# Optimization experiments

Hardware: AMD Instinct MI355X
Metric: run time of the kernel (lower is better)

The kernel has to match this reference:

```python
import jax, jax.numpy as jnp
import numpy as np

B, N, HID, H, DH, NB = 4, 4096, 768, 12, 64, 266
EPS = 1e-4


def softmax_kernel(data, proj, is_query):
    # data: [B,H,N,DH], proj: [NB,DH]. FAVOR+ positive softmax features.
    d = data.shape[-1]
    ratio = proj.shape[0] ** -0.5
    dn = d ** -0.25  # data normalizer
    data_dash = jnp.einsum('bhnd,jd->bhnj', data * dn, proj)  # [B,H,N,NB]
    diag = 0.5 * jnp.sum((data * dn) ** 2, axis=-1, keepdims=True)  # [B,H,N,1]
    if is_query:
        m = jnp.max(data_dash, axis=-1, keepdims=True)
    else:
        m = jnp.max(data_dash, axis=(-1, -2), keepdims=True)
    return ratio * (jnp.exp(data_dash - diag - m) + EPS)


def setup_inputs() -> dict:
    key = jax.random.key(0)
    ks = jax.random.split(key, 8)
    s = HID ** -0.5
    return {
        'hidden_states': jax.random.normal(ks[0], (B, N, HID), jnp.float32),
        'Wq': jax.random.normal(ks[1], (HID, HID), jnp.float32) * s,
        'bq': jnp.zeros((HID,), jnp.float32),
        'Wk': jax.random.normal(ks[2], (HID, HID), jnp.float32) * s,
        'bk': jnp.zeros((HID,), jnp.float32),
        'Wv': jax.random.normal(ks[3], (HID, HID), jnp.float32) * s,
        'bv': jnp.zeros((HID,), jnp.float32),
        'proj': jax.random.normal(ks[4], (NB, DH), jnp.float32),
    }


def reference(hidden_states, Wq, bq, Wk, bk, Wv, bv, proj):
    def heads(x):  # [B,N,HID] -> [B,H,N,DH]
        return x.reshape(B, N, H, DH).transpose(0, 2, 1, 3)

    q = heads(hidden_states @ Wq.T + bq)
    k = heads(hidden_states @ Wk.T + bk)
    v = heads(hidden_states @ Wv.T + bv)

    qp = softmax_kernel(q, proj, True)   # [B,H,N,NB]
    kp = softmax_kernel(k, proj, False)  # [B,H,N,NB]

    # non-causal linear attention: out = q' (k'^T v) / (q' sum_n k')
    k_sum = jnp.sum(kp, axis=2)                               # [B,H,NB]
    d_inv = 1.0 / jnp.einsum('bhnj,bhj->bhn', qp, k_sum)      # [B,H,N]
    ctx = jnp.einsum('bhnj,bhnd->bhjd', kp, v)                # [B,H,NB,DH]
    out = jnp.einsum('bhnj,bhjd->bhnd', qp, ctx) * d_inv[..., None]

    return out.transpose(0, 2, 1, 3).reshape(B, N, HID)
```

## Files before the change

kernel.cpp:

```cpp
#include <hip/hip_runtime.h>
#include <hip/hip_bf16.h>
#include <stdint.h>

#define B_   4
#define N_   4096
#define HID_ 768
#define H_   12
#define DH_  64
#define NB_  266
#define NBP_ 288
#define EPS_ 1e-4f
#define RATIO_ 0.06131393f

typedef unsigned short u16;
typedef __attribute__((ext_vector_type(8))) short short8;
typedef __attribute__((ext_vector_type(4))) float floatx4;

__device__ __forceinline__ u16 f2b(float f) {
  __hip_bfloat16 h = __float2bfloat16(f);
  return *reinterpret_cast<u16*>(&h);
}
__device__ __forceinline__ float b2f(u16 u) {
  union { unsigned u; float f; } x; x.u = ((unsigned)u) << 16; return x.f;
}
__device__ __forceinline__ unsigned fmap(float x) {
  unsigned u = __float_as_uint(x);
  return (u & 0x80000000u) ? ~u : (u | 0x80000000u);
}
__device__ __forceinline__ float funmap(unsigned u) {
  unsigned b = (u & 0x80000000u) ? (u & 0x7FFFFFFFu) : ~u;
  return __uint_as_float(b);
}
__device__ __forceinline__ void gl16(const u16* g, u16* l) {
  __builtin_amdgcn_global_load_lds(
      (const __attribute__((address_space(1))) void*)g,
      (__attribute__((address_space(3))) void*)l, 16, 0, 0);
}

__global__ __launch_bounds__(256) void k_prep(
    const float4* __restrict__ hs, const float4* __restrict__ Wq,
    const float4* __restrict__ Wk, const float4* __restrict__ Wv,
    const float* __restrict__ proj,
    uint2* __restrict__ hsb, uint2* __restrict__ wb3, u16* __restrict__ projb,
    unsigned* __restrict__ mbuf) {
  int blk = blockIdx.x;
  const int t = threadIdx.x;
  if (blk < 12288) {
    int i = blk * 256 + t;
    float4 v = hs[i];
    union { u16 s[4]; uint2 u; } pk;
    pk.s[0] = f2b(v.x); pk.s[1] = f2b(v.y); pk.s[2] = f2b(v.z); pk.s[3] = f2b(v.w);
    hsb[i] = pk.u;
    return;
  }
  blk -= 12288;
  if (blk < 1728) {
    int i = blk * 256 + t;
    int sel = i / 147456, j = i - sel * 147456;
    const float4* s = (sel == 0) ? Wq : (sel == 1) ? Wk : Wv;
    float4 v = s[j];
    union { u16 s4[4]; uint2 u; } pk;
    pk.s4[0] = f2b(v.x); pk.s4[1] = f2b(v.y); pk.s4[2] = f2b(v.z); pk.s4[3] = f2b(v.w);
    wb3[i] = pk.u;
    return;
  }
  blk -= 1728;
  if (blk < 72) {
    int i = blk * 256 + t;
    int j = i / DH_, d = i - j * DH_;
    float v = (j < NB_) ? proj[j * DH_ + d] * 0.35355339059327373f : 0.f;
    projb[i] = f2b(v);
    return;
  }
  blk -= 72;
  if (blk == 0 && t < B_ * H_) mbuf[t] = 0u;
}

__global__ __launch_bounds__(512, 2) void k_qkv2(
    const u16* __restrict__ hsb, const u16* __restrict__ wb,
    const float* __restrict__ bq, const float* __restrict__ bk, const float* __restrict__ bv,
    u16* __restrict__ qb, u16* __restrict__ kb, u16* __restrict__ vT) {
  __shared__ u16 lds[3 * 16384];
  const int orig = blockIdx.x;
  const int lg = (orig & 7) * 72 + (orig >> 3);
  const int tm = lg / 9, tn = lg - tm * 9;
  const int m0 = tm * 256;
  const int c0 = tn * 256;
  const int sel = c0 / 768;
  const int or0 = c0 - sel * 768;
  const u16* W = wb + (size_t)sel * HID_ * HID_;
  const int t = threadIdx.x, lane = t & 63, wv = t >> 6;
  const int lm = lane & 15, lq = lane >> 4;
  const int wvm = wv >> 2, wvn = wv & 3;
  const int srow = t >> 2;
  const int scol = ((t & 3) ^ ((t >> 3) & 3)) * 8;
  const u16* gA0 = hsb + (size_t)(m0 + srow) * HID_ + scol;
  const u16* gB0 = W + (size_t)(or0 + srow) * HID_ + scol;
  u16* lb = lds + wv * 512;
  const int slotc = (lq ^ ((lm >> 1) & 3)) * 8;
  const int aoff = (wvm * 128 + lm) * 32 + slotc;
  const int boff = 8192 + (wvn * 64 + lm) * 32 + slotc;

  floatx4 acc[8][4];
#pragma unroll
  for (int mt = 0; mt < 8; mt++)
#pragma unroll
    for (int nt = 0; nt < 4; nt++) acc[mt][nt] = (floatx4){0.f, 0.f, 0.f, 0.f};

#define STAGE_QKV(kt)                                            \
  {                                                              \
    const int k0_ = (kt) * 32;                                   \
    u16* l_ = lb + ((kt) % 3) * 16384;                           \
    gl16(gA0 + k0_, l_);                                         \
    gl16(gA0 + 128 * HID_ + k0_, l_ + 4096);                     \
    gl16(gB0 + k0_, l_ + 8192);                                  \
    gl16(gB0 + 128 * HID_ + k0_, l_ + 12288);                    \
  }

  STAGE_QKV(0);
  STAGE_QKV(1);
  asm volatile("s_waitcnt vmcnt(4)" ::: "memory");
  __builtin_amdgcn_s_barrier();

  for (int kt = 0; kt < 24; ++kt) {
    if (kt + 2 < 24) STAGE_QKV(kt + 2);
    const u16* bufA = lds + (kt % 3) * 16384;
    short8 af[8], bf[4];
#pragma unroll
    for (int mt = 0; mt < 8; mt++) af[mt] = *(const short8*)&bufA[aoff + mt * 512];
#pragma unroll
    for (int nt = 0; nt < 4; nt++) bf[nt] = *(const short8*)&bufA[boff + nt * 512];
    __builtin_amdgcn_s_setprio(1);
#pragma unroll
    for (int mt = 0; mt < 8; mt++)
#pragma unroll
      for (int nt = 0; nt < 4; nt++)
        acc[mt][nt] = __builtin_amdgcn_mfma_f32_16x16x32_bf16(af[mt], bf[nt], acc[mt][nt], 0, 0, 0);
    __builtin_amdgcn_s_setprio(0);
    if (kt < 22) asm volatile("s_waitcnt vmcnt(4)" ::: "memory");
    else         asm volatile("s_waitcnt vmcnt(0)" ::: "memory");
    __builtin_amdgcn_s_barrier();
  }
#undef STAGE_QKV

  if (sel < 2) {
    const float* bias = (sel == 0) ? bq : bk;
    u16* dst = (sel == 0) ? qb : kb;
#pragma unroll
    for (int nt = 0; nt < 4; nt++) {
      int lc = or0 + wvn * 64 + nt * 16 + lm;
      float bb = bias[lc];
#pragma unroll
      for (int mt = 0; mt < 8; mt++) {
        int rowb = m0 + wvm * 128 + mt * 16 + lq * 4;
#pragma unroll
        for (int r = 0; r < 4; r++)
          dst[(size_t)(rowb + r) * HID_ + lc] = f2b(acc[mt][nt][r] + bb);
      }
    }
  } else {
#pragma unroll
    for (int nt = 0; nt < 4; nt++) {
      int lc = or0 + wvn * 64 + nt * 16 + lm;
      int hh = lc >> 6, dv = lc & 63;
      float bb = bv[lc];
#pragma unroll
      for (int mt = 0; mt < 8; mt++) {
        int rowbase = m0 + wvm * 128 + mt * 16 + lq * 4;
        int b = rowbase >> 12, n = rowbase & 4095;
        union { u16 s[4]; uint2 u; } pk;
#pragma unroll
        for (int r = 0; r < 4; r++) pk.s[r] = f2b(acc[mt][nt][r] + bb);
        *(uint2*)(vT + ((size_t)(b * H_ + hh) * DH_ + dv) * N_ + n) = pk.u;
      }
    }
  }
}

__global__ __launch_bounds__(256) void k_kmax3(
    const u16* __restrict__ kb, const u16* __restrict__ projb,
    unsigned* __restrict__ mbuf, float* __restrict__ diagk) {
  const int bh = blockIdx.y, b = bh / H_, h = bh - b * H_;
  const int n0 = blockIdx.x * 256;
  const int t = threadIdx.x, lane = t & 63, wv = t >> 6;
  const int lm = lane & 15, lq = lane >> 4;
  const u16* kbase = kb + (size_t)(b * N_ + n0 + wv * 64) * HID_ + h * DH_;
  short8 af0[4], af1[4];
#pragma unroll
  for (int mt = 0; mt < 4; mt++) {
    const u16* p = kbase + (size_t)(mt * 16 + lm) * HID_ + lq * 8;
    af0[mt] = *(const short8*)p;
    af1[mt] = *(const short8*)(p + 32);
  }
#pragma unroll
  for (int mt = 0; mt < 4; mt++) {
    float rs = 0.f;
#pragma unroll
    for (int i = 0; i < 8; i++) { float f = b2f(((const u16*)&af0[mt])[i]); rs += f * f; }
#pragma unroll
    for (int i = 0; i < 8; i++) { float f = b2f(((const u16*)&af1[mt])[i]); rs += f * f; }
    rs += __shfl_xor(rs, 16);
    rs += __shfl_xor(rs, 32);
    if (lq == 0) diagk[(size_t)bh * N_ + n0 + wv * 64 + mt * 16 + lm] = 0.0625f * rs;
  }
  float mx = -3e38f;
  for (int ct = 0; ct < 17; ct++) {
    const u16* pp = projb + (ct * 16 + lm) * DH_ + lq * 8;
    short8 bf0 = *(const short8*)pp;
    short8 bf1 = *(const short8*)(pp + 32);
    bool valid = (ct < 16) || (lm < 10);
#pragma unroll
    for (int mt = 0; mt < 4; mt++) {
      floatx4 a = __builtin_amdgcn_mfma_f32_16x16x32_bf16(af0[mt], bf0, (floatx4){0.f,0.f,0.f,0.f}, 0, 0, 0);
      a = __builtin_amdgcn_mfma_f32_16x16x32_bf16(af1[mt], bf1, a, 0, 0, 0);
      if (valid) {
#pragma unroll
        for (int r = 0; r < 4; r++) mx = fmaxf(mx, a[r]);
      }
    }
  }
#pragma unroll
  for (int o = 1; o < 64; o <<= 1) mx = fmaxf(mx, __shfl_xor(mx, o));
  if (lane == 0) atomicMax(&mbuf[bh], fmap(mx));
}

__global__ __launch_bounds__(256) void k_ctx4(
    const u16* __restrict__ kb, const u16* __restrict__ vT, const u16* __restrict__ projb,
    const unsigned* __restrict__ mbuf, const float* __restrict__ diagk,
    float* __restrict__ ksum, u16* __restrict__ ctxb) {
  __shared__ u16 kpl[32 * 72];
  __shared__ float kred[4][2][16];
  const int orig = blockIdx.x;
  const int lg = (orig & 7) * 54 + (orig >> 3);
  const int bh = lg / 9, jb = lg - bh * 9;
  const int j0 = jb * 32;
  const int b = bh / H_, h = bh - b * H_;
  const int t = threadIdx.x, lane = t & 63, wv = t >> 6;
  const int lm = lane & 15, lq = lane >> 4;
  const float m = funmap(mbuf[bh]);
  const bool vj0 = (j0 + lm) < NB_;
  const bool vj1 = (j0 + 16 + lm) < NB_;
  short8 bp00, bp01, bp10, bp11;
  {
    const u16* pp = projb + (j0 + lm) * DH_ + lq * 8;
    bp00 = *(const short8*)pp;
    bp01 = *(const short8*)(pp + 32);
    pp += 16 * DH_;
    bp10 = *(const short8*)pp;
    bp11 = *(const short8*)(pp + 32);
  }
  const u16* kbB = kb + (size_t)(b * N_) * HID_ + h * DH_;
  const u16* vTb = vT + ((size_t)bh * DH_ + wv * 16 + lm) * N_;
  const float* dgB = diagk + (size_t)bh * N_;
  floatx4 acc0 = (floatx4){0.f,0.f,0.f,0.f}, acc1 = (floatx4){0.f,0.f,0.f,0.f};
  float kacc0 = 0.f, kacc1 = 0.f;
  const u16* kr0 = kbB + (size_t)(wv * 16 + lm) * HID_ + lq * 8;
  short8 af0 = *(const short8*)kr0;
  short8 af1 = *(const short8*)(kr0 + 32);
  floatx4 dg4 = *(const floatx4*)(dgB + wv * 16 + lq * 4);

  for (int n64 = 0; n64 < N_; n64 += 64) {
    __syncthreads();
    const int nn = (n64 + 64 < N_) ? n64 + 64 : 0;
    const u16* krn = kbB + (size_t)(nn + wv * 16 + lm) * HID_ + lq * 8;
    short8 nf0 = *(const short8*)krn;
    short8 nf1 = *(const short8*)(krn + 32);
    floatx4 nd = *(const floatx4*)(dgB + nn + wv * 16 + lq * 4);
    short8 av0 = *(const short8*)(vTb + n64 + lq * 8);
    short8 av1 = *(const short8*)(vTb + n64 + 32 + lq * 8);
    {
      floatx4 a = __builtin_amdgcn_mfma_f32_16x16x32_bf16(af0, bp00, (floatx4){0.f,0.f,0.f,0.f}, 0, 0, 0);
      a = __builtin_amdgcn_mfma_f32_16x16x32_bf16(af1, bp01, a, 0, 0, 0);
      union { u16 s[4]; uint2 u; } pk;
      float kss = 0.f;
#pragma unroll
      for (int r = 0; r < 4; r++) {
        float val = vj0 ? RATIO_ * (__expf(a[r] - dg4[r] - m) + EPS_) : 0.f;
        kss += val;
        pk.s[r] = f2b(val);
      }
      kacc0 += kss;
      *(uint2*)&kpl[lm * 72 + wv * 16 + lq * 4] = pk.u;
      a = __builtin_amdgcn_mfma_f32_16x16x32_bf16(af0, bp10, (floatx4){0.f,0.f,0.f,0.f}, 0, 0, 0);
      a = __builtin_amdgcn_mfma_f32_16x16x32_bf16(af1, bp11, a, 0, 0, 0);
      kss = 0.f;
#pragma unroll
      for (int r = 0; r < 4; r++) {
        float val = vj1 ? RATIO_ * (__expf(a[r] - dg4[r] - m) + EPS_) : 0.f;
        kss += val;
        pk.s[r] = f2b(val);
      }
      kacc1 += kss;
      *(uint2*)&kpl[(16 + lm) * 72 + wv * 16 + lq * 4] = pk.u;
    }
    __syncthreads();
    {
      short8 bf = *(const short8*)&kpl[lm * 72 + lq * 8];
      acc0 = __builtin_amdgcn_mfma_f32_16x16x32_bf16(av0, bf, acc0, 0, 0, 0);
      bf = *(const short8*)&kpl[(16 + lm) * 72 + lq * 8];
      acc1 = __builtin_amdgcn_mfma_f32_16x16x32_bf16(av0, bf, acc1, 0, 0, 0);
      bf = *(const short8*)&kpl[lm * 72 + 32 + lq * 8];
      acc0 = __builtin_amdgcn_mfma_f32_16x16x32_bf16(av1, bf, acc0, 0, 0, 0);
      bf = *(const short8*)&kpl[(16 + lm) * 72 + 32 + lq * 8];
      acc1 = __builtin_amdgcn_mfma_f32_16x16x32_bf16(av1, bf, acc1, 0, 0, 0);
    }
    af0 = nf0; af1 = nf1; dg4 = nd;
  }
  {
    float v0 = kacc0; v0 += __shfl_xor(v0, 16); v0 += __shfl_xor(v0, 32);
    float v1 = kacc1; v1 += __shfl_xor(v1, 16); v1 += __shfl_xor(v1, 32);
    if (lq == 0) { kred[wv][0][lm] = v0; kred[wv][1][lm] = v1; }
  }
  __syncthreads();
  if (t < 32) {
    int jh = t >> 4, l = t & 15;
    ksum[bh * NBP_ + j0 + t] =
        kred[0][jh][l] + kred[1][jh][l] + kred[2][jh][l] + kred[3][jh][l];
  }
  {
    u16* cb = ctxb + ((size_t)bh * DH_ + wv * 16 + lq * 4) * NBP_ + j0 + lm;
#pragma unroll
    for (int r = 0; r < 4; r++) {
      cb[(size_t)r * NBP_] = f2b(acc0[r]);
      cb[(size_t)r * NBP_ + 16] = f2b(acc1[r]);
    }
  }
}

__global__ __launch_bounds__(256) void k_out3(
    const u16* __restrict__ qb, const u16* __restrict__ projb,
    const u16* __restrict__ ctxb, const float* __restrict__ ksum,
    float* __restrict__ outp) {
  __shared__ u16 qpl[4][16][296];
  const int bh = blockIdx.y, b = bh / H_, h = bh - b * H_;
  const int n0 = blockIdx.x * 256;
  const int t = threadIdx.x, lane = t & 63, wv = t >> 6;
  const int lm = lane & 15, lq = lane >> 4;
  const u16* qbase = qb + (size_t)(b * N_ + n0 + wv * 64) * HID_ + h * DH_;
  const u16* cb = ctxb + (size_t)bh * DH_ * NBP_;
  const float* ksb = ksum + bh * NBP_;
  float ksv[17];
#pragma unroll
  for (int ct = 0; ct < 17; ct++) ksv[ct] = ksb[ct * 16 + lm];

  for (int mt = 0; mt < 4; mt++) {
    const u16* prow = qbase + (size_t)(mt * 16 + lm) * HID_ + lq * 8;
    short8 af0 = *(const short8*)prow;
    short8 af1 = *(const short8*)(prow + 32);
    float rs = 0.f;
#pragma unroll
    for (int i = 0; i < 8; i++) { float f = b2f(((const u16*)&af0)[i]); rs += f * f; }
#pragma unroll
    for (int i = 0; i < 8; i++) { float f = b2f(((const u16*)&af1)[i]); rs += f * f; }
    rs += __shfl_xor(rs, 16);
    rs += __shfl_xor(rs, 32);
    float dg[4];
#pragma unroll
    for (int r = 0; r < 4; r++) dg[r] = 0.0625f * __shfl(rs, lq * 4 + r);

    float rm[4] = {-3e38f, -3e38f, -3e38f, -3e38f};
#pragma unroll
    for (int ct = 0; ct < 17; ct++) {
      const u16* pp = projb + (ct * 16 + lm) * DH_ + lq * 8;
      short8 bf0 = *(const short8*)pp;
      short8 bf1 = *(const short8*)(pp + 32);
      floatx4 a = __builtin_amdgcn_mfma_f32_16x16x32_bf16(af0, bf0, (floatx4){0.f,0.f,0.f,0.f}, 0, 0, 0);
      a = __builtin_amdgcn_mfma_f32_16x16x32_bf16(af1, bf1, a, 0, 0, 0);
      if ((ct < 16) || (lm < 10)) {
#pragma unroll
        for (int r = 0; r < 4; r++) rm[r] = fmaxf(rm[r], a[r]);
      }
    }
#pragma unroll
    for (int o = 1; o < 16; o <<= 1) {
#pragma unroll
      for (int r = 0; r < 4; r++) rm[r] = fmaxf(rm[r], __shfl_xor(rm[r], o));
    }
    float dpart[4] = {0.f, 0.f, 0.f, 0.f};
#pragma unroll
    for (int ct = 0; ct < 18; ct++) {
      floatx4 a;
      if (ct < 17) {
        const u16* pp = projb + (ct * 16 + lm) * DH_ + lq * 8;
        short8 bf0 = *(const short8*)pp;
        short8 bf1 = *(const short8*)(pp + 32);
        a = __builtin_amdgcn_mfma_f32_16x16x32_bf16(af0, bf0, (floatx4){0.f,0.f,0.f,0.f}, 0, 0, 0);
        a = __builtin_amdgcn_mfma_f32_16x16x32_bf16(af1, bf1, a, 0, 0, 0);
      } else {
        a = (floatx4){0.f, 0.f, 0.f, 0.f};
      }
      bool valid = (ct < 16) || (ct == 16 && lm < 10);
      float kv = (ct < 17) ? ksv[ct] : 0.f;
#pragma unroll
      for (int r = 0; r < 4; r++) {
        float qpv = valid ? RATIO_ * (__expf(a[r] - dg[r] - rm[r]) + EPS_) : 0.f;
        dpart[r] += qpv * kv;
        qpl[wv][lq * 4 + r][ct * 16 + lm] = f2b(qpv);
      }
    }
#pragma unroll
    for (int o = 1; o < 16; o <<= 1) {
#pragma unroll
      for (int r = 0; r < 4; r++) dpart[r] += __shfl_xor(dpart[r], o);
    }
    float dinv[4];
#pragma unroll
    for (int r = 0; r < 4; r++) dinv[r] = 1.f / dpart[r];

    floatx4 ao[4];
#pragma unroll
    for (int dt = 0; dt < 4; dt++) ao[dt] = (floatx4){0.f, 0.f, 0.f, 0.f};
#pragma unroll
    for (int ks9 = 0; ks9 < 9; ks9++) {
      short8 aq = *(const short8*)&qpl[wv][lm][ks9 * 32 + lq * 8];
#pragma unroll
      for (int dt = 0; dt < 4; dt++) {
        short8 bc = *(const short8*)(cb + (size_t)(dt * 16 + lm) * NBP_ + ks9 * 32 + lq * 8);
        ao[dt] = __builtin_amdgcn_mfma_f32_16x16x32_bf16(aq, bc, ao[dt], 0, 0, 0);
      }
    }
#pragma unroll
    for (int dt = 0; dt < 4; dt++) {
#pragma unroll
      for (int r = 0; r < 4; r++) {
        int n = n0 + wv * 64 + mt * 16 + lq * 4 + r;
        outp[((size_t)(b * N_ + n)) * HID_ + h * DH_ + dt * 16 + lm] = ao[dt][r] * dinv[r];
      }
    }
  }
}

extern "C" void kernel_launch(void* const* d_in, const int* in_sizes, int n_in,
                              void* d_out, int out_size, void* d_ws, size_t ws_size,
                              hipStream_t stream) {
  (void)in_sizes; (void)n_in; (void)out_size; (void)ws_size;
  const float* hs   = (const float*)d_in[0];
  const float* Wq   = (const float*)d_in[1];
  const float* bq   = (const float*)d_in[2];
  const float* Wk   = (const float*)d_in[3];
  const float* bk   = (const float*)d_in[4];
  const float* Wv   = (const float*)d_in[5];
  const float* bv   = (const float*)d_in[6];
  const float* proj = (const float*)d_in[7];

  char* w = (char*)d_ws;
  u16* hsb   = (u16*)w;  w += (size_t)16384 * 768 * 2;
  u16* wb3   = (u16*)w;  w += (size_t)3 * 768 * 768 * 2;
  u16* projb = (u16*)w;  w += (size_t)NBP_ * 64 * 2;
  u16* qb    = (u16*)w;  w += (size_t)16384 * 768 * 2;
  u16* kb    = (u16*)w;  w += (size_t)16384 * 768 * 2;
  u16* vT    = (u16*)w;  w += (size_t)48 * DH_ * N_ * 2;
  float* ksum  = (float*)w; w += (size_t)48 * NBP_ * 4;
  float* diagk = (float*)w; w += (size_t)48 * N_ * 4;
  u16* ctxTb = (u16*)w;  w += (size_t)48 * DH_ * NBP_ * 2;
  unsigned* mbuf = (unsigned*)w;

  hipLaunchKernelGGL(k_prep, dim3(14089), dim3(256), 0, stream,
                     (const float4*)hs, (const float4*)Wq, (const float4*)Wk, (const float4*)Wv,
                     proj, (uint2*)hsb, (uint2*)wb3, projb, mbuf);
  hipLaunchKernelGGL(k_qkv2, dim3(576), dim3(512), 0, stream, hsb, wb3, bq, bk, bv, qb, kb, vT);
  hipLaunchKernelGGL(k_kmax3, dim3(16, 48), dim3(256), 0, stream, kb, projb, mbuf, diagk);
  hipLaunchKernelGGL(k_ctx4, dim3(432), dim3(256), 0, stream, kb, vT, projb, mbuf, diagk, ksum, ctxTb);
  hipLaunchKernelGGL(k_out3, dim3(16, 48), dim3(256), 0, stream, qb, projb, ctxTb, ksum, (float*)d_out);
}
```

Measured before the change: 364.4 us.

## Split output kernel per 16-row tile and cache projection scores in registers

The output kernel now processes one 16-row tile per wave instead of looping over four. The grid grows fourfold, giving more blocks and better latency hiding across the GPU. The 17 projection MFMA results are kept in registers from the max pass and reused for the exp pass, instead of being recomputed. This costs more registers (17 floatx4 values) and repeats the per-block ksum load across more blocks, which may reduce occupancy.

Result: slower. 388.6 us (+6.6%).

```diff
diff --git a/kernel.cpp b/kernel.cpp
--- a/kernel.cpp
+++ b/kernel.cpp
@@ -327,105 +327,95 @@
   }
 }
 
-__global__ __launch_bounds__(256) void k_out3(
+__global__ __launch_bounds__(256) void k_out4(
     const u16* __restrict__ qb, const u16* __restrict__ projb,
     const u16* __restrict__ ctxb, const float* __restrict__ ksum,
     float* __restrict__ outp) {
   __shared__ u16 qpl[4][16][296];
   const int bh = blockIdx.y, b = bh / H_, h = bh - b * H_;
-  const int n0 = blockIdx.x * 256;
   const int t = threadIdx.x, lane = t & 63, wv = t >> 6;
   const int lm = lane & 15, lq = lane >> 4;
-  const u16* qbase = qb + (size_t)(b * N_ + n0 + wv * 64) * HID_ + h * DH_;
+  const int row0 = blockIdx.x * 64 + wv * 16;
   const u16* cb = ctxb + (size_t)bh * DH_ * NBP_;
   const float* ksb = ksum + bh * NBP_;
   float ksv[17];
 #pragma unroll
   for (int ct = 0; ct < 17; ct++) ksv[ct] = ksb[ct * 16 + lm];
 
-  for (int mt = 0; mt < 4; mt++) {
-    const u16* prow = qbase + (size_t)(mt * 16 + lm) * HID_ + lq * 8;
-    short8 af0 = *(const short8*)prow;
-    short8 af1 = *(const short8*)(prow + 32);
-    float rs = 0.f;
-#pragma unroll
-    for (int i = 0; i < 8; i++) { float f = b2f(((const u16*)&af0)[i]); rs += f * f; }
-#pragma unroll
-    for (int i = 0; i < 8; i++) { float f = b2f(((const u16*)&af1)[i]); rs += f * f; }
-    rs += __shfl_xor(rs, 16);
-    rs += __shfl_xor(rs, 32);
-    float dg[4];
-#pragma unroll
-    for (int r = 0; r < 4; r++) dg[r] = 0.0625f * __shfl(rs, lq * 4 + r);
-
-    float rm[4] = {-3e38f, -3e38f, -3e38f, -3e38f};
-#pragma unroll
-    for (int ct = 0; ct < 17; ct++) {
-      const u16* pp = projb + (ct * 16 + lm) * DH_ + lq * 8;
-      short8 bf0 = *(const short8*)pp;
-      short8 bf1 = *(const short8*)(pp + 32);
-      floatx4 a = __builtin_amdgcn_mfma_f32_16x16x32_bf16(af0, bf0, (floatx4){0.f,0.f,0.f,0.f}, 0, 0, 0);
-      a = __builtin_amdgcn_mfma_f32_16x16x32_bf16(af1, bf1, a, 0, 0, 0);
-      if ((ct < 16) || (lm < 10)) {
-#pragma unroll
-        for (int r = 0; r < 4; r++) rm[r] = fmaxf(rm[r], a[r]);
-      }
-    }
-#pragma unroll
-    for (int o = 1; o < 16; o <<= 1) {
-#pragma unroll
-      for (int r = 0; r < 4; r++) rm[r] = fmaxf(rm[r], __shfl_xor(rm[r], o));
-    }
-    float dpart[4] = {0.f, 0.f, 0.f, 0.f};
-#pragma unroll
-    for (int ct = 0; ct < 18; ct++) {
-      floatx4 a;
-      if (ct < 17) {
-        const u16* pp = projb + (ct * 16 + lm) * DH_ + lq * 8;
-        short8 bf0 = *(const short8*)pp;
-        short8 bf1 = *(const short8*)(pp + 32);
-        a = __builtin_amdgcn_mfma_f32_16x16x32_bf16(af0, bf0, (floatx4){0.f,0.f,0.f,0.f}, 0, 0, 0);
-        a = __builtin_amdgcn_mfma_f32_16x16x32_bf16(af1, bf1, a, 0, 0, 0);
-      } else {
-        a = (floatx4){0.f, 0.f, 0.f, 0.f};
-      }
-      bool valid = (ct < 16) || (ct == 16 && lm < 10);
-      float kv = (ct < 17) ? ksv[ct] : 0.f;
-#pragma unroll
-      for (int r = 0; r < 4; r++) {
-        float qpv = valid ? RATIO_ * (__expf(a[r] - dg[r] - rm[r]) + EPS_) : 0.f;
-        dpart[r] += qpv * kv;
-        qpl[wv][lq * 4 + r][ct * 16 + lm] = f2b(qpv);
-      }
-    }
-#pragma unroll
-    for (int o = 1; o < 16; o <<= 1) {
-#pragma unroll
-      for (int r = 0; r < 4; r++) dpart[r] += __shfl_xor(dpart[r], o);
-    }
-    float dinv[4];
-#pragma unroll
-    for (int r = 0; r < 4; r++) dinv[r] = 1.f / dpart[r];
-
-    floatx4 ao[4];
-#pragma unroll
-    for (int dt = 0; dt < 4; dt++) ao[dt] = (floatx4){0.f, 0.f, 0.f, 0.f};
-#pragma unroll
-    for (int ks9 = 0; ks9 < 9; ks9++) {
-      short8 aq = *(const short8*)&qpl[wv][lm][ks9 * 32 + lq * 8];
-#pragma unroll
-      for (int dt = 0; dt < 4; dt++) {
-        short8 bc = *(const short8*)(cb + (size_t)(dt * 16 + lm) * NBP_ + ks9 * 32 + lq * 8);
-        ao[dt] = __builtin_amdgcn_mfma_f32_16x16x32_bf16(aq, bc, ao[dt], 0, 0, 0);
-      }
-    }
+  const u16* prow = qb + (size_t)(b * N_ + row0 + lm) * HID_ + h * DH_ + lq * 8;
+  short8 af0 = *(const short8*)prow;
+  short8 af1 = *(const short8*)(prow + 32);
+  float rs = 0.f;
+#pragma unroll
+  for (int i = 0; i < 8; i++) { float f = b2f(((const u16*)&af0)[i]); rs += f * f; }
+#pragma unroll
+  for (int i = 0; i < 8; i++) { float f = b2f(((const u16*)&af1)[i]); rs += f * f; }
+  rs += __shfl_xor(rs, 16);
+  rs += __shfl_xor(rs, 32);
+  float dg[4];
+#pragma unroll
+  for (int r = 0; r < 4; r++) dg[r] = 0.0625f * __shfl(rs, lq * 4 + r);
+
+  floatx4 dd[17];
+  float rm[4] = {-3e38f, -3e38f, -3e38f, -3e38f};
+#pragma unroll
+  for (int ct = 0; ct < 17; ct++) {
+    const u16* pp = projb + (ct * 16 + lm) * DH_ + lq * 8;
+    short8 bf0 = *(const short8*)pp;
+    short8 bf1 = *(const short8*)(pp + 32);
+    floatx4 a = __builtin_amdgcn_mfma_f32_16x16x32_bf16(af0, bf0, (floatx4){0.f,0.f,0.f,0.f}, 0, 0, 0);
+    a = __builtin_amdgcn_mfma_f32_16x16x32_bf16(af1, bf1, a, 0, 0, 0);
+    dd[ct] = a;
+    if ((ct < 16) || (lm < 10)) {
+#pragma unroll
+      for (int r = 0; r < 4; r++) rm[r] = fmaxf(rm[r], a[r]);
+    }
+  }
+#pragma unroll
+  for (int o = 1; o < 16; o <<= 1) {
+#pragma unroll
+    for (int r = 0; r < 4; r++) rm[r] = fmaxf(rm[r], __shfl_xor(rm[r], o));
+  }
+  float dpart[4] = {0.f, 0.f, 0.f, 0.f};
+#pragma unroll
+  for (int ct = 0; ct < 17; ct++) {
+    bool valid = (ct < 16) || (lm < 10);
+#pragma unroll
+    for (int r = 0; r < 4; r++) {
+      float qpv = valid ? RATIO_ * (__expf(dd[ct][r] - dg[r] - rm[r]) + EPS_) : 0.f;
+      dpart[r] += qpv * ksv[ct];
+      qpl[wv][lq * 4 + r][ct * 16 + lm] = f2b(qpv);
+    }
+  }
+#pragma unroll
+  for (int r = 0; r < 4; r++) qpl[wv][lq * 4 + r][272 + lm] = 0;
+#pragma unroll
+  for (int o = 1; o < 16; o <<= 1) {
+#pragma unroll
+    for (int r = 0; r < 4; r++) dpart[r] += __shfl_xor(dpart[r], o);
+  }
+  float dinv[4];
+#pragma unroll
+  for (int r = 0; r < 4; r++) dinv[r] = 1.f / dpart[r];
+
+  floatx4 ao[4];
+#pragma unroll
+  for (int dt = 0; dt < 4; dt++) ao[dt] = (floatx4){0.f, 0.f, 0.f, 0.f};
+#pragma unroll
+  for (int ks9 = 0; ks9 < 9; ks9++) {
+    short8 aq = *(const short8*)&qpl[wv][lm][ks9 * 32 + lq * 8];
 #pragma unroll
     for (int dt = 0; dt < 4; dt++) {
-#pragma unroll
-      for (int r = 0; r < 4; r++) {
-        int n = n0 + wv * 64 + mt * 16 + lq * 4 + r;
-        outp[((size_t)(b * N_ + n)) * HID_ + h * DH_ + dt * 16 + lm] = ao[dt][r] * dinv[r];
-      }
+      short8 bc = *(const short8*)(cb + (size_t)(dt * 16 + lm) * NBP_ + ks9 * 32 + lq * 8);
+      ao[dt] = __builtin_amdgcn_mfma_f32_16x16x32_bf16(aq, bc, ao[dt], 0, 0, 0);
+    }
+  }
+#pragma unroll
+  for (int dt = 0; dt < 4; dt++) {
+#pragma unroll
+    for (int r = 0; r < 4; r++) {
+      int n = row0 + lq * 4 + r;
+      outp[((size_t)(b * N_ + n)) * HID_ + h * DH_ + dt * 16 + lm] = ao[dt][r] * dinv[r];
     }
   }
 }
@@ -461,5 +451,5 @@
   hipLaunchKernelGGL(k_qkv2, dim3(576), dim3(512), 0, stream, hsb, wb3, bq, bk, bv, qb, kb, vT);
   hipLaunchKernelGGL(k_kmax3, dim3(16, 48), dim3(256), 0, stream, kb, projb, mbuf, diagk);
   hipLaunchKernelGGL(k_ctx4, dim3(432), dim3(256), 0, stream, kb, vT, projb, mbuf, diagk, ksum, ctxTb);
-  hipLaunchKernelGGL(k_out3, dim3(16, 48), dim3(256), 0, stream, qb, projb, ctxTb, ksum, (float*)d_out);
-}
+  hipLaunchKernelGGL(k_out4, dim3(64, 48), dim3(256), 0, stream, qb, projb, ctxTb, ksum, (float*)d_out);
+}
```
